# Performance work log

Measured on AMD Instinct MI355X. Metric: run time of the kernel, lower is better.

Reference implementation:

```python
import jax, jax.numpy as jnp
import numpy as np

N = 8192
F_IN = 256
F_OUT = 256
EDGE_P = 0.005  # graph density, avg degree ~41


def setup_inputs() -> dict:
    key = jax.random.key(0)
    k_x, k_adj, k_w, k_phi = jax.random.split(key, 4)
    x = jax.random.normal(k_x, (N, F_IN), dtype=jnp.float32)
    adj = (jax.random.uniform(k_adj, (N, N)) < EDGE_P).astype(jnp.float32)
    stdv_w = 1.0 / np.sqrt(F_OUT)  # torch uses weight.size(1)
    weight = jax.random.uniform(k_w, (F_IN, F_OUT), minval=-stdv_w, maxval=stdv_w, dtype=jnp.float32)
    bias = jnp.zeros((F_OUT,), dtype=jnp.float32)
    stdv_phi = 1.0  # 1/sqrt(phi.size(1)=1)
    phi = jax.random.uniform(k_phi, (2 * F_OUT, 1), minval=-stdv_phi, maxval=stdv_phi, dtype=jnp.float32)
    return {"adj": adj, "x": x, "weight": weight, "bias": bias, "phi": phi}


def reference(adj, x, weight, bias, phi):
    n = x.shape[0]
    H = x @ weight + bias  # [N, F]
    # S[i,j] = phi^T [H_i ; H_j] -> additive decomposition, no [N*N, 2F] concat
    f = H.shape[1]
    s_src = H @ phi[:f, 0]  # [N], contribution of row node i
    s_dst = H @ phi[f:, 0]  # [N], contribution of col node j
    S = s_src[:, None] + s_dst[None, :]  # [N, N]
    mask = (adj + jnp.eye(n, dtype=adj.dtype)) != 0
    S_masked = jnp.where(mask, S, -jnp.inf)
    attn = jax.nn.softmax(S_masked, axis=1)  # diag always unmasked -> no nan rows
    h = attn @ H  # [N, F]
    return jax.nn.leaky_relu(h, negative_slope=0.01)
```

## Files before the change

### kernel.cpp

```cpp
#include <hip/hip_runtime.h>
#include <hip/hip_bf16.h>

typedef __attribute__((ext_vector_type(8))) short short8;
typedef __attribute__((ext_vector_type(4))) float f32x4;

#define N_NODES 8192
#define F 256
#define MAXDEG 1024

static __device__ __forceinline__ unsigned short f2bf(float f) {
    unsigned int u = __builtin_bit_cast(unsigned int, f);
    u += 0x7FFFu + ((u >> 16) & 1u);
    return (unsigned short)(u >> 16);
}
static __device__ __forceinline__ float bf2f(unsigned short h) {
    unsigned int u = ((unsigned int)h) << 16;
    return __builtin_bit_cast(float, u);
}

__global__ __launch_bounds__(256) void k_prep(const float* __restrict__ W,
                                              unsigned short* __restrict__ Wt) {
    int k = blockIdx.x;
    int n = threadIdx.x;
    Wt[n * 256 + k] = f2bf(W[k * 256 + n]);
}

__global__ __launch_bounds__(256) void k_gemm(const float* __restrict__ x,
                                              const float* __restrict__ bias,
                                              const float* __restrict__ phi,
                                              const unsigned short* __restrict__ Wt,
                                              unsigned short* __restrict__ H,
                                              float* __restrict__ s_dst) {
    const int tid  = threadIdx.x;
    const int wave = tid >> 6;
    const int lane = tid & 63;
    const int lrow = lane & 15;
    const int lk   = lane >> 4;
    const int r0   = blockIdx.x * 64 + wave * 16;

    f32x4 acc[16];
#pragma unroll
    for (int n = 0; n < 16; ++n) acc[n] = (f32x4){0.f, 0.f, 0.f, 0.f};

#pragma unroll
    for (int k0 = 0; k0 < 256; k0 += 32) {
        const float* ap = x + (size_t)(r0 + lrow) * 256 + k0 + lk * 8;
        float4 a0 = *(const float4*)ap;
        float4 a1 = *(const float4*)(ap + 4);
        short8 a;
        a[0] = (short)f2bf(a0.x); a[1] = (short)f2bf(a0.y);
        a[2] = (short)f2bf(a0.z); a[3] = (short)f2bf(a0.w);
        a[4] = (short)f2bf(a1.x); a[5] = (short)f2bf(a1.y);
        a[6] = (short)f2bf(a1.z); a[7] = (short)f2bf(a1.w);
#pragma unroll
        for (int n = 0; n < 16; ++n) {
            short8 b = *(const short8*)(Wt + (size_t)(n * 16 + lrow) * 256 + k0 + lk * 8);
            acc[n] = __builtin_amdgcn_mfma_f32_16x16x32_bf16(a, b, acc[n], 0, 0, 0);
        }
    }

    float sd[4] = {0.f, 0.f, 0.f, 0.f};
#pragma unroll
    for (int n = 0; n < 16; ++n) {
        int c = n * 16 + lrow;
        float bv = bias[c];
        float ph = phi[256 + c];
#pragma unroll
        for (int i = 0; i < 4; ++i) {
            int r = r0 + lk * 4 + i;
            float h = acc[n][i] + bv;
            H[(size_t)r * 256 + c] = f2bf(h);
            sd[i] += h * ph;
        }
    }
#pragma unroll
    for (int m = 1; m < 16; m <<= 1) {
#pragma unroll
        for (int i = 0; i < 4; ++i) sd[i] += __shfl_xor(sd[i], m, 64);
    }
    if (lrow == 0) {
#pragma unroll
        for (int i = 0; i < 4; ++i) s_dst[r0 + lk * 4 + i] = sd[i];
    }
}

__global__ __launch_bounds__(256) void k_attn(const float* __restrict__ adj,
                                              const unsigned short* __restrict__ H,
                                              const float* __restrict__ s_dst,
                                              float* __restrict__ out) {
    __shared__ int   s_idx[MAXDEG];
    __shared__ float s_w[MAXDEG];
    __shared__ int   s_cnt;
    __shared__ float s_red[8];

    const int i   = blockIdx.x;
    const int tid = threadIdx.x;
    if (tid == 0) s_cnt = 0;
    __syncthreads();

    const float4* arow = (const float4*)(adj + (size_t)i * N_NODES);
#pragma unroll
    for (int c = 0; c < 8; ++c) {
        int v4 = c * 256 + tid;
        float4 v = arow[v4];
        int col = v4 * 4;
        float vv[4] = {v.x, v.y, v.z, v.w};
#pragma unroll
        for (int j = 0; j < 4; ++j) {
            if (vv[j] != 0.f || (col + j) == i) {
                int p = atomicAdd(&s_cnt, 1);
                if (p < MAXDEG) s_idx[p] = col + j;
            }
        }
    }
    __syncthreads();
    const int cnt = min(s_cnt, MAXDEG);

    float mv = -3e38f;
    for (int t = tid; t < cnt; t += 256) {
        float sv = s_dst[s_idx[t]];
        s_w[t] = sv;
        mv = fmaxf(mv, sv);
    }
#pragma unroll
    for (int d = 32; d; d >>= 1) mv = fmaxf(mv, __shfl_xor(mv, d, 64));
    if ((tid & 63) == 0) s_red[tid >> 6] = mv;
    __syncthreads();
    mv = fmaxf(fmaxf(s_red[0], s_red[1]), fmaxf(s_red[2], s_red[3]));
    __syncthreads();

    float zv = 0.f;
    for (int t = tid; t < cnt; t += 256) {
        float w = __expf(s_w[t] - mv);
        s_w[t] = w;
        zv += w;
    }
#pragma unroll
    for (int d = 32; d; d >>= 1) zv += __shfl_xor(zv, d, 64);
    if ((tid & 63) == 0) s_red[4 + (tid >> 6)] = zv;
    __syncthreads();
    zv = (s_red[4] + s_red[5]) + (s_red[6] + s_red[7]);
    const float zinv = 1.0f / zv;

    float acc = 0.f;
#pragma unroll 4
    for (int t = 0; t < cnt; ++t) {
        acc = fmaf(s_w[t], bf2f(H[(size_t)s_idx[t] * F + tid]), acc);
    }
    float h = acc * zinv;
    out[(size_t)i * F + tid] = (h >= 0.f) ? h : 0.01f * h;
}

extern "C" void kernel_launch(void* const* d_in, const int* in_sizes, int n_in,
                              void* d_out, int out_size, void* d_ws, size_t ws_size,
                              hipStream_t stream) {
    const float* adj  = (const float*)d_in[0];
    const float* x    = (const float*)d_in[1];
    const float* W    = (const float*)d_in[2];
    const float* bias = (const float*)d_in[3];
    const float* phi  = (const float*)d_in[4];
    float* out = (float*)d_out;

    char* ws = (char*)d_ws;
    unsigned short* Wt = (unsigned short*)ws;
    unsigned short* H  = (unsigned short*)(ws + (131072));
    float* s_dst       = (float*)(ws + 131072 + 4194304);

    hipLaunchKernelGGL(k_prep, dim3(256),     dim3(256), 0, stream, W, Wt);
    hipLaunchKernelGGL(k_gemm, dim3(N_NODES / 64), dim3(256), 0, stream,
                       x, bias, phi, Wt, H, s_dst);
    hipLaunchKernelGGL(k_attn, dim3(N_NODES), dim3(256), 0, stream,
                       adj, H, s_dst, out);
}
```

Before: 402.3 us.

## Assign one wave per attention row with vectorized bf16 gathers

The attention kernel now processes four rows per block, one per wave, so softmax reductions use only wave shuffles and no block-level barriers or shared reduction arrays. Each lane gathers four consecutive bf16 features per neighbour with a short4 load and writes a float4 output, which cuts the number of gather instructions. Atomic appends are skipped when a float4 chunk has no edges. The per-row neighbour cap drops from 1024 to 256, which holds for the expected degree of about 41 but would silently truncate much denser rows.

```diff
diff --git a/kernel.cpp b/kernel.cpp
--- a/kernel.cpp
+++ b/kernel.cpp
@@ -6,7 +6,6 @@
 
 #define N_NODES 8192
 #define F 256
-#define MAXDEG 1024
 
 static __device__ __forceinline__ unsigned short f2bf(float f) {
     unsigned int u = __builtin_bit_cast(unsigned int, f);
@@ -84,71 +83,87 @@
     }
 }
 
+#define CAP 256
 __global__ __launch_bounds__(256) void k_attn(const float* __restrict__ adj,
                                               const unsigned short* __restrict__ H,
                                               const float* __restrict__ s_dst,
                                               float* __restrict__ out) {
-    __shared__ int   s_idx[MAXDEG];
-    __shared__ float s_w[MAXDEG];
-    __shared__ int   s_cnt;
-    __shared__ float s_red[8];
+    __shared__ int   s_idx[4][CAP];
+    __shared__ float s_w[4][CAP];
+    __shared__ int   s_cnt[4];
 
-    const int i   = blockIdx.x;
-    const int tid = threadIdx.x;
-    if (tid == 0) s_cnt = 0;
+    const int tid  = threadIdx.x;
+    const int wave = tid >> 6;
+    const int lane = tid & 63;
+    const int i    = (blockIdx.x << 2) | wave;
+
+    if (lane == 0) s_cnt[wave] = 0;
     __syncthreads();
 
-    const float4* arow = (const float4*)(adj + (size_t)i * N_NODES);
-#pragma unroll
-    for (int c = 0; c < 8; ++c) {
-        int v4 = c * 256 + tid;
+    const float4* __restrict__ arow = (const float4*)(adj + (size_t)i * N_NODES);
+#pragma unroll 4
+    for (int c = 0; c < 32; ++c) {
+        int v4 = (c << 6) | lane;
         float4 v = arow[v4];
-        int col = v4 * 4;
+        int col = v4 << 2;
         float vv[4] = {v.x, v.y, v.z, v.w};
+        bool act[4];
+        bool any = false;
 #pragma unroll
         for (int j = 0; j < 4; ++j) {
-            if (vv[j] != 0.f || (col + j) == i) {
-                int p = atomicAdd(&s_cnt, 1);
-                if (p < MAXDEG) s_idx[p] = col + j;
+            act[j] = (vv[j] != 0.f) || ((col + j) == i);
+            any |= act[j];
+        }
+        if (any) {
+#pragma unroll
+            for (int j = 0; j < 4; ++j) {
+                if (act[j]) {
+                    int p = atomicAdd(&s_cnt[wave], 1);
+                    if (p < CAP) s_idx[wave][p] = col + j;
+                }
             }
         }
     }
-    __syncthreads();
-    const int cnt = min(s_cnt, MAXDEG);
+    int cnt = min(s_cnt[wave], CAP);
 
     float mv = -3e38f;
-    for (int t = tid; t < cnt; t += 256) {
-        float sv = s_dst[s_idx[t]];
-        s_w[t] = sv;
+    for (int t = lane; t < cnt; t += 64) {
+        float sv = s_dst[s_idx[wave][t]];
+        s_w[wave][t] = sv;
         mv = fmaxf(mv, sv);
     }
 #pragma unroll
     for (int d = 32; d; d >>= 1) mv = fmaxf(mv, __shfl_xor(mv, d, 64));
-    if ((tid & 63) == 0) s_red[tid >> 6] = mv;
-    __syncthreads();
-    mv = fmaxf(fmaxf(s_red[0], s_red[1]), fmaxf(s_red[2], s_red[3]));
-    __syncthreads();
 
     float zv = 0.f;
-    for (int t = tid; t < cnt; t += 256) {
-        float w = __expf(s_w[t] - mv);
-        s_w[t] = w;
+    for (int t = lane; t < cnt; t += 64) {
+        float w = __expf(s_w[wave][t] - mv);
+        s_w[wave][t] = w;
         zv += w;
     }
 #pragma unroll
     for (int d = 32; d; d >>= 1) zv += __shfl_xor(zv, d, 64);
-    if ((tid & 63) == 0) s_red[4 + (tid >> 6)] = zv;
-    __syncthreads();
-    zv = (s_red[4] + s_red[5]) + (s_red[6] + s_red[7]);
     const float zinv = 1.0f / zv;
 
-    float acc = 0.f;
+    float a0 = 0.f, a1 = 0.f, a2 = 0.f, a3 = 0.f;
+    const unsigned short* __restrict__ hb = H + (lane << 2);
 #pragma unroll 4
     for (int t = 0; t < cnt; ++t) {
-        acc = fmaf(s_w[t], bf2f(H[(size_t)s_idx[t] * F + tid]), acc);
+        int   j = s_idx[wave][t];
+        float w = s_w[wave][t];
+        short4 hv = *(const short4*)(hb + (size_t)j * F);
+        a0 = fmaf(w, bf2f((unsigned short)hv.x), a0);
+        a1 = fmaf(w, bf2f((unsigned short)hv.y), a1);
+        a2 = fmaf(w, bf2f((unsigned short)hv.z), a2);
+        a3 = fmaf(w, bf2f((unsigned short)hv.w), a3);
     }
-    float h = acc * zinv;
-    out[(size_t)i * F + tid] = (h >= 0.f) ? h : 0.01f * h;
+    float4 o;
+    o.x = a0 * zinv; o.y = a1 * zinv; o.z = a2 * zinv; o.w = a3 * zinv;
+    o.x = (o.x >= 0.f) ? o.x : 0.01f * o.x;
+    o.y = (o.y >= 0.f) ? o.y : 0.01f * o.y;
+    o.z = (o.z >= 0.f) ? o.z : 0.01f * o.z;
+    o.w = (o.w >= 0.f) ? o.w : 0.01f * o.w;
+    *(float4*)(out + (size_t)i * F + (lane << 2)) = o;
 }
 
 extern "C" void kernel_launch(void* const* d_in, const int* in_sizes, int n_in,
@@ -166,9 +181,9 @@
     unsigned short* H  = (unsigned short*)(ws + (131072));
     float* s_dst       = (float*)(ws + 131072 + 4194304);
 
-    hipLaunchKernelGGL(k_prep, dim3(256),     dim3(256), 0, stream, W, Wt);
+    hipLaunchKernelGGL(k_prep, dim3(256),          dim3(256), 0, stream, W, Wt);
     hipLaunchKernelGGL(k_gemm, dim3(N_NODES / 64), dim3(256), 0, stream,
                        x, bias, phi, Wt, H, s_dst);
-    hipLaunchKernelGGL(k_attn, dim3(N_NODES), dim3(256), 0, stream,
+    hipLaunchKernelGGL(k_attn, dim3(N_NODES / 4),  dim3(256), 0, stream,
                        adj, H, s_dst, out);
 }
```

Measured after the change: 399.7 us. About the same (-0.6%).
